# Kernel optimization log

Hardware: AMD Instinct MI355X
Metric: run time of the kernel (lower is better)

## Reference

```python
import jax, jax.numpy as jnp
import numpy as np

D_MODEL = 1024
D_STATE = 64
D_HEAD = 64
N_HEADS = 16
D_INNER = D_HEAD * N_HEADS  # 1024
K = 4  # conv kernel size
BATCH = 4
SEQ = 4096
LN_EPS = 1e-5


def setup_inputs() -> dict:
    key = jax.random.key(0)
    k0, k1, k2, k3, k4 = jax.random.split(key, 5)
    x = jax.random.normal(k0, (BATCH, SEQ, D_MODEL), jnp.float32)
    # nn.Linear(d_model, 2*d_inner + 2*d_state, bias=False): weight (out, in)
    in_proj_w = jax.random.normal(k1, (2 * D_INNER + 2 * D_STATE, D_MODEL), jnp.float32) / np.sqrt(D_MODEL).astype(np.float32)
    # depthwise Conv1d: weight (d_inner, 1, K), bias (d_inner,)
    conv_w = jax.random.normal(k2, (D_INNER, 1, K), jnp.float32) * 0.5
    conv_b = jax.random.normal(k3, (D_INNER,), jnp.float32) * 0.1
    # _init_parameters: A = -log(arange(1..d_state)) broadcast to (H, Dh, N)
    A_param = jnp.broadcast_to(-jnp.log(jnp.arange(1, D_STATE + 1, dtype=jnp.float32))[None, None, :],
                               (N_HEADS, D_HEAD, D_STATE))
    ln_w = jnp.ones((D_INNER,), jnp.float32)
    ln_b = jnp.zeros((D_INNER,), jnp.float32)
    out_proj_w = jax.random.normal(k4, (D_MODEL, D_INNER), jnp.float32) / np.sqrt(D_INNER).astype(np.float32)
    return {"x": x, "in_proj_w": in_proj_w, "conv_w": conv_w, "conv_b": conv_b,
            "A_param": A_param, "ln_w": ln_w, "ln_b": ln_b, "out_proj_w": out_proj_w}


def _ssd_scan(xh, Bm, Cm, A_param):
    # xh: (B, L, H, Dh); Bm, Cm: (B, L, N)
    A_disc = jnp.exp(-jnp.exp(A_param))  # (H, Dh, N)

    def step(h, inp):
        x_t, B_t, C_t = inp  # (B,H,Dh), (B,N), (B,N)
        h = h * A_disc + B_t[:, None, None, :] * x_t[..., None]  # (B,H,Dh,N)
        y_t = jnp.einsum('bhdn,bn->bhd', h, C_t)
        return h, y_t

    b = xh.shape[0]
    h0 = jnp.zeros((b, N_HEADS, D_HEAD, D_STATE), xh.dtype)
    xs = (jnp.swapaxes(xh, 0, 1), jnp.swapaxes(Bm, 0, 1), jnp.swapaxes(Cm, 0, 1))
    _, ys = jax.lax.scan(step, h0, xs)  # ys: (L, B, H, Dh)
    return jnp.swapaxes(ys, 0, 1)  # (B, L, H, Dh)


def reference(x, in_proj_w, conv_w, conv_b, A_param, ln_w, ln_b, out_proj_w):
    b, L, _ = x.shape
    xBC = x @ in_proj_w.T  # (B, L, 2*d_inner + 2*d_state)
    xc = xBC[..., :D_INNER]
    z = xBC[..., D_INNER:2 * D_INNER]
    Bm = xBC[..., 2 * D_INNER:2 * D_INNER + D_STATE]
    Cm = xBC[..., 2 * D_INNER + D_STATE:]
    # causal depthwise conv (padding=3 then truncate == left-pad K-1)
    xt = jnp.swapaxes(xc, 1, 2)  # (B, C, L)
    y = jax.lax.conv_general_dilated(xt, conv_w, window_strides=(1,), padding=[(K - 1, 0)],
                                     feature_group_count=D_INNER,
                                     dimension_numbers=('NCH', 'OIH', 'NCH'))
    xc = jnp.swapaxes(y + conv_b[None, :, None], 1, 2)  # (B, L, d_inner)
    xc = jax.nn.silu(xc)
    xh = xc.reshape(b, L, N_HEADS, D_HEAD)
    yssd = _ssd_scan(xh, Bm, Cm, A_param).reshape(b, L, D_INNER)
    yg = yssd * jax.nn.silu(z)
    mu = yg.mean(-1, keepdims=True)
    var = yg.var(-1, keepdims=True)
    yn = (yg - mu) / jnp.sqrt(var + LN_EPS) * ln_w + ln_b
    return yn @ out_proj_w.T
```

## Files before the change

kernel.cpp:

```cpp
#include <hip/hip_runtime.h>

typedef unsigned short u16;
typedef unsigned int u32;
typedef __attribute__((ext_vector_type(8))) short bf16x8;
typedef __attribute__((ext_vector_type(4))) float f32x4;

#define BATCH 4
#define SEQ 4096
#define DMODEL 1024
#define DINNER 1024
#define NPROJ 2176
#define MROWS (BATCH*SEQ)
#define NCHUNK 64
#define CLEN 64
#define NPAD 2304

__device__ __forceinline__ float bf2f(u16 u) {
    union { u32 i; float f; } v; v.i = ((u32)u) << 16; return v.f;
}
__device__ __forceinline__ u16 f2bf(float f) {
    union { float f; u32 i; } v; v.f = f;
    u32 r = v.i + 0x7FFFu + ((v.i >> 16) & 1u);
    return (u16)(r >> 16);
}
__device__ __forceinline__ float silu_f(float x) { return x / (1.0f + expf(-x)); }

__device__ __forceinline__ void gload8f(const u16* p, float* o) {
    bf16x8 v = *(const bf16x8*)p;
    #pragma unroll
    for (int j = 0; j < 8; ++j) o[j] = bf2f((u16)v[j]);
}

__device__ __forceinline__ void ld_lds16(const u16* g, u16* l) {
    __builtin_amdgcn_global_load_lds(
        (const __attribute__((address_space(1))) u32*)g,
        (__attribute__((address_space(3))) u32*)l, 16, 0, 0);
}

__global__ __launch_bounds__(256) void cast_f2b(
    const float* __restrict__ src, u16* __restrict__ dst, int n8)
{
    int i = blockIdx.x * 256 + threadIdx.x;
    if (i >= n8) return;
    size_t o = (size_t)i * 8;
    float4 a = *(const float4*)(src + o);
    float4 b = *(const float4*)(src + o + 4);
    u16 v[8] = {f2bf(a.x), f2bf(a.y), f2bf(a.z), f2bf(a.w),
                f2bf(b.x), f2bf(b.y), f2bf(b.z), f2bf(b.w)};
    *(bf16x8*)(dst + o) = *(bf16x8*)v;
}

__global__ __launch_bounds__(256) void cast_w1p_k(
    const float* __restrict__ src, u16* __restrict__ dst)
{
    int i = blockIdx.x * 256 + threadIdx.x;
    int row = i >> 7;
    size_t o = (size_t)i * 8;
    u16 v[8];
    if (row < NPROJ) {
        float4 a = *(const float4*)(src + o);
        float4 b = *(const float4*)(src + o + 4);
        v[0]=f2bf(a.x); v[1]=f2bf(a.y); v[2]=f2bf(a.z); v[3]=f2bf(a.w);
        v[4]=f2bf(b.x); v[5]=f2bf(b.y); v[6]=f2bf(b.z); v[7]=f2bf(b.w);
    } else {
        #pragma unroll
        for (int j = 0; j < 8; ++j) v[j] = 0;
    }
    *(bf16x8*)(dst + o) = *(bf16x8*)v;
}

__global__ __launch_bounds__(256) void tables_k(
    const float* __restrict__ A_param, float* __restrict__ l2a_g,
    float* __restrict__ apw, float* __restrict__ ainv)
{
    __shared__ float l2s[64];
    int tid = threadIdx.x;
    if (tid < 64) {
        float v = -expf(A_param[tid]) * 1.44269504088896340736f;
        l2s[tid] = v;
        l2a_g[tid] = v;
    }
    __syncthreads();
    #pragma unroll
    for (int i = 0; i < 16; ++i) {
        int e = tid * 16 + i;
        int t = e >> 6, n = e & 63;
        float x = (float)t * l2s[n];
        apw[e]  = exp2f(x);
        ainv[e] = exp2f(-x);
    }
}

#define GK 1024
#define GNT 16

template<typename TO, int GN, int NV, int LDC>
__global__ __launch_bounds__(512, 2) void gemm8p_k(
    const u16* __restrict__ A, const u16* __restrict__ B, TO* __restrict__ C)
{
    __shared__ u16 lds[65536];

    const int cpx = (GN * 64) >> 3;
    const int bid = blockIdx.x;
    const int swz = (bid & 7) * cpx + (bid >> 3);
    const int bm = swz / GN, bn = swz % GN;
    const int m0 = bm * 256, n0 = bn * 256;

    const int tid = threadIdx.x;
    const int wid = tid >> 6, lane = tid & 63;
    const int wm = wid >> 2, wn = wid & 3;
    const int quad = lane >> 4, l16 = lane & 15;
    const int xsw = (l16 & 7) << 3;

    u16* L = lds;
    const u16* Ab = A + (size_t)m0 * GK;
    const u16* Bb = B + (size_t)n0 * GK;

    auto stage = [&](const u16* gbase, u16* ldsb) {
        {
            int c = tid;
            int row = c >> 3, slot = (c & 7) ^ (row & 7);
            ld_lds16(gbase + (size_t)row * GK + slot * 8,
                     ldsb + ((tid & ~63) << 3));
        }
        {
            int c = 512 + tid;
            int row = c >> 3, slot = (c & 7) ^ (row & 7);
            ld_lds16(gbase + (size_t)row * GK + slot * 8,
                     ldsb + ((512 + (tid & ~63)) << 3));
        }
    };
    auto rdfrag = [&](const u16* base, int rh, int kh) -> bf16x8 {
        return *(const bf16x8*)(base + rh * 64 + ((kh * 32 + quad * 8) ^ xsw));
    };

    bf16x8 aLo[4][2], aHi[4][2], bLo[2][2], bHi[2][2];
    f32x4 acc[8][4] = {};

    stage(Ab,                     L);
    stage(Ab + 128 * GK,          L + 8192);
    stage(Bb,                     L + 32768);
    stage(Bb + 128 * GK,          L + 40960);
    stage(Ab + 64,                L + 16384);
    stage(Ab + 128 * GK + 64,     L + 24576);
    asm volatile("s_waitcnt vmcnt(4)" ::: "memory");
    __builtin_amdgcn_s_barrier();
    {
        const u16* Ard = L + wm * 8192;
        #pragma unroll
        for (int i = 0; i < 4; ++i)
            #pragma unroll
            for (int kh = 0; kh < 2; ++kh)
                aLo[i][kh] = rdfrag(Ard, i * 16 + l16, kh);
    }

    for (int t = 0; t < GNT; ++t) {
        const int cb = t & 1;
        u16* Acur = L + cb * 16384;
        u16* Anxt = L + (cb ^ 1) * 16384;
        u16* Bnxt = L + 32768 + (cb ^ 1) * 16384;
        const u16* ArdC = Acur + wm * 8192;
        const u16* ArdN = Anxt + wm * 8192;
        const u16* BrdC = L + 32768 + cb * 16384 + (wn >> 1) * 8192;
        const int brh = (wn & 1) * 64;

        #pragma unroll
        for (int j = 0; j < 2; ++j)
            #pragma unroll
            for (int kh = 0; kh < 2; ++kh)
                bLo[j][kh] = rdfrag(BrdC, brh + j * 16 + l16, kh);
        if (t + 1 < GNT) stage(Bb + (t + 1) * 64, Bnxt);
        __builtin_amdgcn_s_barrier();
        asm volatile("s_waitcnt lgkmcnt(0)" ::: "memory");
        __builtin_amdgcn_s_setprio(1);
        #pragma unroll
        for (int kh = 0; kh < 2; ++kh)
            #pragma unroll
            for (int i = 0; i < 4; ++i)
                #pragma unroll
                for (int j = 0; j < 2; ++j)
                    acc[i][j] = __builtin_amdgcn_mfma_f32_16x16x32_bf16(
                        aLo[i][kh], bLo[j][kh], acc[i][j], 0, 0, 0);
        __builtin_amdgcn_s_setprio(0);
        __builtin_amdgcn_s_barrier();

        #pragma unroll
        for (int j = 0; j < 2; ++j)
            #pragma unroll
            for (int kh = 0; kh < 2; ++kh)
                bHi[j][kh] = rdfrag(BrdC, brh + 32 + j * 16 + l16, kh);
        if (t + 1 < GNT) stage(Bb + 128 * GK + (t + 1) * 64, Bnxt + 8192);
        __builtin_amdgcn_s_barrier();
        asm volatile("s_waitcnt lgkmcnt(0)" ::: "memory");
        __builtin_amdgcn_s_setprio(1);
        #pragma unroll
        for (int kh = 0; kh < 2; ++kh)
            #pragma unroll
            for (int i = 0; i < 4; ++i)
                #pragma unroll
                for (int j = 0; j < 2; ++j)
                    acc[i][2 + j] = __builtin_amdgcn_mfma_f32_16x16x32_bf16(
                        aLo[i][kh], bHi[j][kh], acc[i][2 + j], 0, 0, 0);
        __builtin_amdgcn_s_setprio(0);
        __builtin_amdgcn_s_barrier();

        #pragma unroll
        for (int i = 0; i < 4; ++i)
            #pragma unroll
            for (int kh = 0; kh < 2; ++kh)
                aHi[i][kh] = rdfrag(ArdC, 64 + i * 16 + l16, kh);
        if (t + 2 < GNT) stage(Ab + (t + 2) * 64, Acur);
        if (t + 2 < GNT)      { asm volatile("s_waitcnt vmcnt(6)" ::: "memory"); }
        else if (t + 1 < GNT) { asm volatile("s_waitcnt vmcnt(4)" ::: "memory"); }
        __builtin_amdgcn_s_barrier();
        asm volatile("s_waitcnt lgkmcnt(0)" ::: "memory");
        __builtin_amdgcn_s_setprio(1);
        #pragma unroll
        for (int kh = 0; kh < 2; ++kh)
            #pragma unroll
            for (int i = 0; i < 4; ++i)
                #pragma unroll
                for (int j = 0; j < 2; ++j)
                    acc[4 + i][2 + j] = __builtin_amdgcn_mfma_f32_16x16x32_bf16(
                        aHi[i][kh], bHi[j][kh], acc[4 + i][2 + j], 0, 0, 0);
        __builtin_amdgcn_s_setprio(0);
        __builtin_amdgcn_s_barrier();

        if (t + 1 < GNT) {
            #pragma unroll
            for (int i = 0; i < 4; ++i)
                #pragma unroll
                for (int kh = 0; kh < 2; ++kh)
                    aLo[i][kh] = rdfrag(ArdN, i * 16 + l16, kh);
        }
        if (t + 2 < GNT) stage(Ab + 128 * GK + (t + 2) * 64, Acur + 8192);
        if (t + 2 < GNT)      { asm volatile("s_waitcnt vmcnt(4)" ::: "memory"); }
        else if (t + 1 < GNT) { asm volatile("s_waitcnt vmcnt(0)" ::: "memory"); }
        __builtin_amdgcn_s_barrier();
        asm volatile("s_waitcnt lgkmcnt(0)" ::: "memory");
        __builtin_amdgcn_s_setprio(1);
        #pragma unroll
        for (int kh = 0; kh < 2; ++kh)
            #pragma unroll
            for (int i = 0; i < 4; ++i)
                #pragma unroll
                for (int j = 0; j < 2; ++j)
                    acc[4 + i][j] = __builtin_amdgcn_mfma_f32_16x16x32_bf16(
                        aHi[i][kh], bLo[j][kh], acc[4 + i][j], 0, 0, 0);
        __builtin_amdgcn_s_setprio(0);
        __builtin_amdgcn_s_barrier();
    }

    __syncthreads();
    if constexpr (sizeof(TO) == 2) {
        u16* eld = lds;
        #pragma unroll
        for (int i = 0; i < 8; ++i)
            #pragma unroll
            for (int j = 0; j < 4; ++j)
                #pragma unroll
                for (int r = 0; r < 4; ++r)
                    eld[(size_t)(wm * 128 + i * 16 + quad * 4 + r) * 256 +
                        wn * 64 + j * 16 + l16] = f2bf(acc[i][j][r]);
        __syncthreads();
        #pragma unroll
        for (int rep = 0; rep < 16; ++rep) {
            int cc = rep * 512 + tid;
            int row = cc >> 5, c8 = (cc & 31) * 8;
            if (n0 + c8 < NV)
                *(bf16x8*)(C + (size_t)(m0 + row) * LDC + n0 + c8) =
                    *(const bf16x8*)(eld + (size_t)row * 256 + c8);
        }
    } else {
        float* eldf = (float*)lds;
        #pragma unroll
        for (int h = 0; h < 2; ++h) {
            if (wm == h) {
                #pragma unroll
                for (int i = 0; i < 8; ++i)
                    #pragma unroll
                    for (int j = 0; j < 4; ++j)
                        #pragma unroll
                        for (int r = 0; r < 4; ++r)
                            eldf[(size_t)(i * 16 + quad * 4 + r) * 256 +
                                 wn * 64 + j * 16 + l16] = acc[i][j][r];
            }
            __syncthreads();
            #pragma unroll
            for (int rep = 0; rep < 16; ++rep) {
                int cc = rep * 512 + tid;
                int row = cc >> 6, c4 = (cc & 63) * 4;
                *(float4*)(C + (size_t)(m0 + h * 128 + row) * LDC + n0 + c4) =
                    *(const float4*)(eldf + (size_t)row * 256 + c4);
            }
            __syncthreads();
        }
    }
}

#define CRPT 8
__global__ __launch_bounds__(256) void conv_k(
    const u16* __restrict__ xBC, const float* __restrict__ conv_w,
    const float* __restrict__ conv_b, u16* __restrict__ xact)
{
    int o = blockIdx.x * 256 + threadIdx.x;
    int c0 = (o & 127) * 8;
    int rg = o >> 7;
    int row0 = rg * CRPT;
    int l0 = row0 & (SEQ - 1);

    float4 wv[8];
    #pragma unroll
    for (int j = 0; j < 8; ++j)
        wv[j] = *(const float4*)(conv_w + (c0 + j) * 4);
    float bias[8];
    {
        float4 b0 = *(const float4*)(conv_b + c0);
        float4 b1 = *(const float4*)(conv_b + c0 + 4);
        bias[0]=b0.x; bias[1]=b0.y; bias[2]=b0.z; bias[3]=b0.w;
        bias[4]=b1.x; bias[5]=b1.y; bias[6]=b1.z; bias[7]=b1.w;
    }

    float win[3][8];
    #pragma unroll
    for (int k = 0; k < 3; ++k) {
        if (l0 - 3 + k < 0) {
            #pragma unroll
            for (int j = 0; j < 8; ++j) win[k][j] = 0.f;
        } else {
            gload8f(xBC + (size_t)(row0 - 3 + k) * NPROJ + c0, win[k]);
        }
    }
    #pragma unroll
    for (int r = 0; r < CRPT; ++r) {
        float cur[8];
        gload8f(xBC + (size_t)(row0 + r) * NPROJ + c0, cur);
        u16 outv[8];
        #pragma unroll
        for (int j = 0; j < 8; ++j) {
            float acc = bias[j]
                + win[0][j] * wv[j].x + win[1][j] * wv[j].y
                + win[2][j] * wv[j].z + cur[j]    * wv[j].w;
            outv[j] = f2bf(silu_f(acc));
        }
        *(bf16x8*)(xact + (size_t)(row0 + r) * DINNER + c0) = *(bf16x8*)outv;
        #pragma unroll
        for (int j = 0; j < 8; ++j) {
            win[0][j] = win[1][j]; win[1][j] = win[2][j]; win[2][j] = cur[j];
        }
    }
}

__global__ __launch_bounds__(256) void ssd_intra_k(
    const u16* __restrict__ xact, u16* __restrict__ xBC,
    u16* __restrict__ Sh, const float* __restrict__ apw,
    const float* __restrict__ ainv)
{
    __shared__ u16 Pl[64][72];
    __shared__ u16 Ql[64][72];
    __shared__ u16 Gl[64][72];
    __shared__ u16 Qt[64][72];
    __shared__ u16 Xt[64][72];

    const int dg = blockIdx.x, c = blockIdx.y, b = blockIdx.z;
    const int dcol = dg * 64;
    const int l0 = c * CLEN;
    const int tid = threadIdx.x;
    const int w = tid >> 6, lane = tid & 63;
    const int quad = lane >> 4, l16 = lane & 15;
    const int tstrip = 16 * w;

    {
        const int st_t = tid >> 3, st_n8 = (tid & 7) * 8;
        #pragma unroll
        for (int rep = 0; rep < 2; ++rep) {
            int t = rep * 32 + st_t;
            size_t row = (size_t)(b * SEQ + l0 + t) * NPROJ;
            float Bv[8], Cv[8];
            gload8f(xBC + row + 2048 + st_n8, Bv);
            gload8f(xBC + row + 2112 + st_n8, Cv);
            float4 aw0 = *(const float4*)&apw[t * 64 + st_n8];
            float4 aw1 = *(const float4*)&apw[t * 64 + st_n8 + 4];
            float4 ai0 = *(const float4*)&ainv[t * 64 + st_n8];
            float4 ai1 = *(const float4*)&ainv[t * 64 + st_n8 + 4];
            float4 ar0 = *(const float4*)&apw[(63 - t) * 64 + st_n8];
            float4 ar1 = *(const float4*)&apw[(63 - t) * 64 + st_n8 + 4];
            float aw[8] = {aw0.x,aw0.y,aw0.z,aw0.w,aw1.x,aw1.y,aw1.z,aw1.w};
            float ai[8] = {ai0.x,ai0.y,ai0.z,ai0.w,ai1.x,ai1.y,ai1.z,ai1.w};
            float ar[8] = {ar0.x,ar0.y,ar0.z,ar0.w,ar1.x,ar1.y,ar1.z,ar1.w};
            u16 p8[8], q8[8];
            #pragma unroll
            for (int j = 0; j < 8; ++j) {
                p8[j] = f2bf(Cv[j] * aw[j]);
                q8[j] = f2bf(Bv[j] * ai[j]);
            }
            *(bf16x8*)&Pl[t][st_n8] = *(bf16x8*)p8;
            *(bf16x8*)&Ql[t][st_n8] = *(bf16x8*)q8;
            #pragma unroll
            for (int j = 0; j < 8; ++j)
                Qt[st_n8 + j][t] = f2bf(Bv[j] * ar[j]);
        }
    }
    {
        #pragma unroll
        for (int rep = 0; rep < 2; ++rep) {
            int idx = rep * 256 + tid;
            int xt_t = idx >> 3, xt_d8 = (idx & 7) * 8;
            float xv[8];
            gload8f(xact + (size_t)(b * SEQ + l0 + xt_t) * DINNER + dcol + xt_d8, xv);
            #pragma unroll
            for (int j = 0; j < 8; ++j) Xt[xt_d8 + j][xt_t] = f2bf(xv[j]);
        }
    }
    __syncthreads();

    bf16x8 af0 = *(const bf16x8*)&Pl[tstrip + l16][0  + quad * 8];
    bf16x8 af1 = *(const bf16x8*)&Pl[tstrip + l16][32 + quad * 8];
    f32x4 g[4] = {};
    #pragma unroll
    for (int j4 = 0; j4 < 4; ++j4) {
        bf16x8 b0 = *(const bf16x8*)&Ql[j4 * 16 + l16][0  + quad * 8];
        bf16x8 b1 = *(const bf16x8*)&Ql[j4 * 16 + l16][32 + quad * 8];
        g[j4] = __builtin_amdgcn_mfma_f32_16x16x32_bf16(af0, b0, g[j4], 0, 0, 0);
        g[j4] = __builtin_amdgcn_mfma_f32_16x16x32_bf16(af1, b1, g[j4], 0, 0, 0);
    }
    __syncthreads();

    #pragma unroll
    for (int j4 = 0; j4 < 4; ++j4) {
        #pragma unroll
        for (int r = 0; r < 4; ++r) {
            int t = tstrip + quad * 4 + r;
            int s = j4 * 16 + l16;
            float val = (s <= t) ? g[j4][r] : 0.f;
            u16 hi = f2bf(val);
            Ql[t][s] = hi;
            Gl[t][s] = f2bf(val - bf2f(hi));
        }
    }
    __syncthreads();

    bf16x8 gh0 = *(const bf16x8*)&Ql[tstrip + l16][0  + quad * 8];
    bf16x8 gh1 = *(const bf16x8*)&Ql[tstrip + l16][32 + quad * 8];
    bf16x8 gl0 = *(const bf16x8*)&Gl[tstrip + l16][0  + quad * 8];
    bf16x8 gl1 = *(const bf16x8*)&Gl[tstrip + l16][32 + quad * 8];
    bf16x8 qt0 = *(const bf16x8*)&Qt[tstrip + l16][0  + quad * 8];
    bf16x8 qt1 = *(const bf16x8*)&Qt[tstrip + l16][32 + quad * 8];

    #pragma unroll
    for (int dt = 0; dt < 4; ++dt) {
        bf16x8 x0 = *(const bf16x8*)&Xt[dt * 16 + l16][0  + quad * 8];
        bf16x8 x1 = *(const bf16x8*)&Xt[dt * 16 + l16][32 + quad * 8];
        f32x4 y = {};
        y = __builtin_amdgcn_mfma_f32_16x16x32_bf16(gh0, x0, y, 0, 0, 0);
        y = __builtin_amdgcn_mfma_f32_16x16x32_bf16(gh1, x1, y, 0, 0, 0);
        y = __builtin_amdgcn_mfma_f32_16x16x32_bf16(gl0, x0, y, 0, 0, 0);
        y = __builtin_amdgcn_mfma_f32_16x16x32_bf16(gl1, x1, y, 0, 0, 0);
        f32x4 s4 = {};
        s4 = __builtin_amdgcn_mfma_f32_16x16x32_bf16(qt0, x0, s4, 0, 0, 0);
        s4 = __builtin_amdgcn_mfma_f32_16x16x32_bf16(qt1, x1, s4, 0, 0, 0);
        #pragma unroll
        for (int r = 0; r < 4; ++r) {
            int t = tstrip + quad * 4 + r;
            xBC[(size_t)(b * SEQ + l0 + t) * NPROJ + dcol + dt * 16 + l16] = f2bf(y[r]);
            int n = tstrip + quad * 4 + r;
            Sh[((size_t)((b * NCHUNK + c) * 64 + n)) * 1024 + dcol + dt * 16 + l16] = f2bf(s4[r]);
        }
    }
}

__global__ __launch_bounds__(256) void state_scan_k(
    u16* __restrict__ Sh, const float* __restrict__ l2a)
{
    int gid = blockIdx.x * 256 + threadIdx.x;
    int b = gid >> 16, r = gid & 65535, n = r >> 10;
    float a64 = exp2f(64.f * l2a[n]);
    float v = 0.f;
    size_t base = ((size_t)b << 22) + r;
    for (int c = 0; c < NCHUNK; ++c) {
        size_t addr = base + ((size_t)c << 16);
        float s = bf2f(Sh[addr]);
        Sh[addr] = f2bf(v);
        v = fmaf(v, a64, s);
    }
}

__global__ __launch_bounds__(512, 2) void inter_gate_k(
    const u16* __restrict__ xBC, const u16* __restrict__ Sh,
    const float* __restrict__ apw, const float* __restrict__ l2a,
    const float* __restrict__ ln_w, const float* __restrict__ ln_b,
    u16* __restrict__ yn)
{
    __shared__ u16 Pl[64][72];
    __shared__ u16 Vt[1024][68];
    __shared__ float red[64][8][2];
    __shared__ float stats[64][2];

    const int c = blockIdx.x, b = blockIdx.y;
    const int tid = threadIdx.x;
    const int w = tid >> 6, lane = tid & 63;
    const int quad = lane >> 4, l16 = lane & 15;
    const int dW = w * 128;
    const int brow = b * SEQ + c * CLEN;

    {
        const int st_t = tid >> 3, st_n8 = (tid & 7) * 8;
        float Cv[8];
        gload8f(xBC + (size_t)(brow + st_t) * NPROJ + 2112 + st_n8, Cv);
        float4 aw0 = *(const float4*)&apw[st_t * 64 + st_n8];
        float4 aw1 = *(const float4*)&apw[st_t * 64 + st_n8 + 4];
        float aw[8] = {aw0.x,aw0.y,aw0.z,aw0.w,aw1.x,aw1.y,aw1.z,aw1.w};
        u16 p8[8];
        #pragma unroll
        for (int j = 0; j < 8; ++j)
            p8[j] = f2bf(Cv[j] * aw[j] * exp2f(l2a[st_n8 + j]));
        *(bf16x8*)&Pl[st_t][st_n8] = *(bf16x8*)p8;
    }
    {
        const size_t vbase = (size_t)((b * NCHUNK + c) * 64) * 1024;
        const int n0 = (tid & 7) * 8;
        #pragma unroll
        for (int rep = 0; rep < 2; ++rep) {
            int d_blk = (tid >> 3) + rep * 64;
            bf16x8 vin[8];
            #pragma unroll
            for (int jj = 0; jj < 8; ++jj)
                vin[jj] = *(const bf16x8*)&Sh[vbase + (size_t)(n0 + jj) * 1024 + d_blk * 8];
            #pragma unroll
            for (int jj2 = 0; jj2 < 8; ++jj2) {
                u16 outv[8];
                #pragma unroll
                for (int jj = 0; jj < 8; ++jj) outv[jj] = (u16)vin[jj][jj2];
                *(bf16x8*)&Vt[d_blk * 8 + jj2][n0] = *(bf16x8*)outv;
            }
        }
    }
    __syncthreads();

    bf16x8 pa[4][2];
    #pragma unroll
    for (int i = 0; i < 4; ++i)
        #pragma unroll
        for (int kh = 0; kh < 2; ++kh)
            pa[i][kh] = *(const bf16x8*)&Pl[i * 16 + l16][kh * 32 + quad * 8];

    f32x4 acc[4][8] = {};
    #pragma unroll
    for (int j = 0; j < 8; ++j) {
        bf16x8 pb0 = *(const bf16x8*)&Vt[dW + j * 16 + l16][quad * 8];
        bf16x8 pb1 = *(const bf16x8*)&Vt[dW + j * 16 + l16][32 + quad * 8];
        #pragma unroll
        for (int i = 0; i < 4; ++i) {
            acc[i][j] = __builtin_amdgcn_mfma_f32_16x16x32_bf16(pa[i][0], pb0, acc[i][j], 0, 0, 0);
            acc[i][j] = __builtin_amdgcn_mfma_f32_16x16x32_bf16(pa[i][1], pb1, acc[i][j], 0, 0, 0);
        }
    }

    float s1[4][4] = {}, s2[4][4] = {};
    #pragma unroll
    for (int i = 0; i < 4; ++i)
        #pragma unroll
        for (int j = 0; j < 8; ++j)
            #pragma unroll
            for (int r = 0; r < 4; ++r) {
                int t = i * 16 + quad * 4 + r;
                size_t rb = (size_t)(brow + t) * NPROJ;
                int d = dW + j * 16 + l16;
                float yo = bf2f(xBC[rb + d]);
                float zz = bf2f(xBC[rb + 1024 + d]);
                float gq = (yo + acc[i][j][r]) * silu_f(zz);
                acc[i][j][r] = gq;
                s1[i][r] += gq;
                s2[i][r] += gq * gq;
            }

    #pragma unroll
    for (int i = 0; i < 4; ++i)
        #pragma unroll
        for (int r = 0; r < 4; ++r) {
            float a = s1[i][r], q = s2[i][r];
            #pragma unroll
            for (int off = 1; off < 16; off <<= 1) {
                a += __shfl_xor(a, off);
                q += __shfl_xor(q, off);
            }
            if (l16 == 0) {
                int t = i * 16 + quad * 4 + r;
                red[t][w][0] = a;
                red[t][w][1] = q;
            }
        }
    __syncthreads();
    if (tid < 64) {
        float ts = 0.f, tq = 0.f;
        #pragma unroll
        for (int ww = 0; ww < 8; ++ww) { ts += red[tid][ww][0]; tq += red[tid][ww][1]; }
        float mu = ts * (1.0f / DINNER);
        float var = tq * (1.0f / DINNER) - mu * mu;
        stats[tid][0] = mu;
        stats[tid][1] = rsqrtf(var + 1e-5f);
    }
    __syncthreads();

    float lw[8], lb[8];
    #pragma unroll
    for (int j = 0; j < 8; ++j) {
        lw[j] = ln_w[dW + j * 16 + l16];
        lb[j] = ln_b[dW + j * 16 + l16];
    }
    #pragma unroll
    for (int i = 0; i < 4; ++i)
        #pragma unroll
        for (int r = 0; r < 4; ++r) {
            int t = i * 16 + quad * 4 + r;
            float mu = stats[t][0], inv = stats[t][1];
            size_t ob = (size_t)(brow + t) * DINNER;
            #pragma unroll
            for (int j = 0; j < 8; ++j) {
                int d = dW + j * 16 + l16;
                yn[ob + d] = f2bf((acc[i][j][r] - mu) * inv * lw[j] + lb[j]);
            }
        }
}

extern "C" void kernel_launch(void* const* d_in, const int* in_sizes, int n_in,
                              void* d_out, int out_size, void* d_ws, size_t ws_size,
                              hipStream_t stream) {
    const float* x   = (const float*)d_in[0];
    const float* w1  = (const float*)d_in[1];
    const float* cw  = (const float*)d_in[2];
    const float* cb  = (const float*)d_in[3];
    const float* ap  = (const float*)d_in[4];
    const float* lnw = (const float*)d_in[5];
    const float* lnb = (const float*)d_in[6];
    const float* w2  = (const float*)d_in[7];
    float* out = (float*)d_out;

    u16* xBC   = (u16*)d_ws;
    u16* xact  = xBC + (size_t)MROWS * NPROJ;
    u16* x_bf  = xact;
    u16* w2_bf = xact + (size_t)MROWS * DINNER;
    float* l2a  = (float*)(w2_bf + (size_t)DMODEL * DINNER);
    float* apw  = l2a + 64;
    float* ainv = apw + 4096;
    u16* w1p = (u16*)d_out;
    u16* Sh  = (u16*)d_out;

    cast_f2b<<<(MROWS * DMODEL / 8) / 256, 256, 0, stream>>>(x, x_bf, MROWS * DMODEL / 8);
    cast_w1p_k<<<(NPAD * DMODEL / 8) / 256, 256, 0, stream>>>(w1, w1p);
    cast_f2b<<<(DMODEL * DINNER / 8) / 256, 256, 0, stream>>>(w2, w2_bf, DMODEL * DINNER / 8);
    tables_k<<<1, 256, 0, stream>>>(ap, l2a, apw, ainv);

    gemm8p_k<u16, 9, NPROJ, NPROJ><<<9 * 64, 512, 0, stream>>>(x_bf, w1p, xBC);
    conv_k<<<(MROWS / CRPT * 128) / 256, 256, 0, stream>>>(xBC, cw, cb, xact);

    ssd_intra_k<<<dim3(16, NCHUNK, BATCH), 256, 0, stream>>>(xact, xBC, Sh, apw, ainv);
    state_scan_k<<<1024, 256, 0, stream>>>(Sh, l2a);
    inter_gate_k<<<dim3(NCHUNK, BATCH), 512, 0, stream>>>(xBC, Sh, apw, l2a, lnw, lnb, xact);

    gemm8p_k<float, 4, DMODEL, DMODEL><<<4 * 64, 512, 0, stream>>>(xact, w2_bf, out);
}
```

Measured before the change: 428.2 us.

## Stage inter-chunk output through LDS for vectorized row-wise gate and LayerNorm

The MFMA accumulator tile is written into shared memory (reusing the Vt buffer, with an XOR swizzle) so that each thread then handles a contiguous row segment. The xBC/z loads and the yn stores become 16-byte vector accesses instead of scattered 2-byte ones. The cross-wave LayerNorm reduction shrinks to an 8-lane shuffle with no red/stats arrays. The launch bound is relaxed to one block per SM. The inter-chunk contribution is rounded to bf16 before the gate, which adds some rounding error, and occupancy may drop.

Measured after the change: 487.0 us. +13.7%, slower.

```diff
diff --git a/kernel.cpp b/kernel.cpp
--- a/kernel.cpp
+++ b/kernel.cpp
@@ -485,7 +485,7 @@
     }
 }
 
-__global__ __launch_bounds__(512, 2) void inter_gate_k(
+__global__ __launch_bounds__(512, 1) void inter_gate_k(
     const u16* __restrict__ xBC, const u16* __restrict__ Sh,
     const float* __restrict__ apw, const float* __restrict__ l2a,
     const float* __restrict__ ln_w, const float* __restrict__ ln_b,
@@ -493,8 +493,6 @@
 {
     __shared__ u16 Pl[64][72];
     __shared__ u16 Vt[1024][68];
-    __shared__ float red[64][8][2];
-    __shared__ float stats[64][2];
 
     const int c = blockIdx.x, b = blockIdx.y;
     const int tid = threadIdx.x;
@@ -502,6 +500,7 @@
     const int quad = lane >> 4, l16 = lane & 15;
     const int dW = w * 128;
     const int brow = b * SEQ + c * CLEN;
+    u16* Lc = &Vt[0][0];
 
     {
         const int st_t = tid >> 3, st_n8 = (tid & 7) * 8;
@@ -555,8 +554,8 @@
             acc[i][j] = __builtin_amdgcn_mfma_f32_16x16x32_bf16(pa[i][1], pb1, acc[i][j], 0, 0, 0);
         }
     }
-
-    float s1[4][4] = {}, s2[4][4] = {};
+    __syncthreads();
+
     #pragma unroll
     for (int i = 0; i < 4; ++i)
         #pragma unroll
@@ -564,63 +563,59 @@
             #pragma unroll
             for (int r = 0; r < 4; ++r) {
                 int t = i * 16 + quad * 4 + r;
-                size_t rb = (size_t)(brow + t) * NPROJ;
                 int d = dW + j * 16 + l16;
-                float yo = bf2f(xBC[rb + d]);
-                float zz = bf2f(xBC[rb + 1024 + d]);
-                float gq = (yo + acc[i][j][r]) * silu_f(zz);
-                acc[i][j][r] = gq;
-                s1[i][r] += gq;
-                s2[i][r] += gq * gq;
+                Lc[t * 1040 + (d ^ (quad << 4))] = f2bf(acc[i][j][r]);
             }
-
-    #pragma unroll
-    for (int i = 0; i < 4; ++i)
-        #pragma unroll
-        for (int r = 0; r < 4; ++r) {
-            float a = s1[i][r], q = s2[i][r];
-            #pragma unroll
-            for (int off = 1; off < 16; off <<= 1) {
-                a += __shfl_xor(a, off);
-                q += __shfl_xor(q, off);
-            }
-            if (l16 == 0) {
-                int t = i * 16 + quad * 4 + r;
-                red[t][w][0] = a;
-                red[t][w][1] = q;
-            }
-        }
-    __syncthreads();
-    if (tid < 64) {
-        float ts = 0.f, tq = 0.f;
-        #pragma unroll
-        for (int ww = 0; ww < 8; ++ww) { ts += red[tid][ww][0]; tq += red[tid][ww][1]; }
-        float mu = ts * (1.0f / DINNER);
-        float var = tq * (1.0f / DINNER) - mu * mu;
-        stats[tid][0] = mu;
-        stats[tid][1] = rsqrtf(var + 1e-5f);
-    }
-    __syncthreads();
-
-    float lw[8], lb[8];
-    #pragma unroll
-    for (int j = 0; j < 8; ++j) {
-        lw[j] = ln_w[dW + j * 16 + l16];
-        lb[j] = ln_b[dW + j * 16 + l16];
-    }
-    #pragma unroll
-    for (int i = 0; i < 4; ++i)
-        #pragma unroll
-        for (int r = 0; r < 4; ++r) {
-            int t = i * 16 + quad * 4 + r;
-            float mu = stats[t][0], inv = stats[t][1];
-            size_t ob = (size_t)(brow + t) * DINNER;
-            #pragma unroll
-            for (int j = 0; j < 8; ++j) {
-                int d = dW + j * 16 + l16;
-                yn[ob + d] = f2bf((acc[i][j][r] - mu) * inv * lw[j] + lb[j]);
-            }
-        }
+    __syncthreads();
+
+    const int row = tid >> 3, c8 = tid & 7;
+    const int qx = ((row >> 2) & 3) << 4;
+    const size_t rb = (size_t)(brow + row) * NPROJ;
+    u16* Lrow = Lc + row * 1040;
+    float s1 = 0.f, s2 = 0.f;
+    #pragma unroll
+    for (int k = 0; k < 16; ++k) {
+        int d0 = c8 * 8 + k * 64;
+        float yv[8], zv[8], cv[8];
+        gload8f(xBC + rb + d0, yv);
+        gload8f(xBC + rb + 1024 + d0, zv);
+        gload8f(Lrow + (d0 ^ qx), cv);
+        u16 g8[8];
+        #pragma unroll
+        for (int jj = 0; jj < 8; ++jj) {
+            float g = (yv[jj] + cv[jj]) * silu_f(zv[jj]);
+            s1 += g; s2 += g * g;
+            g8[jj] = f2bf(g);
+        }
+        *(bf16x8*)(Lrow + (d0 ^ qx)) = *(bf16x8*)g8;
+    }
+    #pragma unroll
+    for (int off = 1; off < 8; off <<= 1) {
+        s1 += __shfl_xor(s1, off);
+        s2 += __shfl_xor(s2, off);
+    }
+    float mu = s1 * (1.0f / DINNER);
+    float var = s2 * (1.0f / DINNER) - mu * mu;
+    float inv = rsqrtf(var + 1e-5f);
+
+    const size_t ob = (size_t)(brow + row) * DINNER;
+    #pragma unroll
+    for (int k = 0; k < 16; ++k) {
+        int d0 = c8 * 8 + k * 64;
+        float gv[8];
+        gload8f(Lrow + (d0 ^ qx), gv);
+        float4 w0 = *(const float4*)(ln_w + d0);
+        float4 w1 = *(const float4*)(ln_w + d0 + 4);
+        float4 b0 = *(const float4*)(ln_b + d0);
+        float4 b1 = *(const float4*)(ln_b + d0 + 4);
+        float lw[8] = {w0.x,w0.y,w0.z,w0.w,w1.x,w1.y,w1.z,w1.w};
+        float lb[8] = {b0.x,b0.y,b0.z,b0.w,b1.x,b1.y,b1.z,b1.w};
+        u16 o8[8];
+        #pragma unroll
+        for (int jj = 0; jj < 8; ++jj)
+            o8[jj] = f2bf((gv[jj] - mu) * inv * lw[jj] + lb[jj]);
+        *(bf16x8*)(yn + ob + d0) = *(bf16x8*)o8;
+    }
 }
 
 extern "C" void kernel_launch(void* const* d_in, const int* in_sizes, int n_in,
```
